# Optimization experiments

Measured on AMD Instinct MI355X. Metric: run time of the kernel, lower is better.

Reference implementation:

```python
import jax, jax.numpy as jnp
import numpy as np

B, N_IN, N_OUT = 8192, 2048, 2048


def setup_inputs() -> dict:
    key = jax.random.key(0)
    kx, kw = jax.random.split(key)
    x = jax.random.normal(kx, (B, N_IN), dtype=jnp.float32)
    # torch: uniform_(-0.5, 0.5)
    weight = jax.random.uniform(kw, (N_IN, N_OUT), dtype=jnp.float32, minval=-0.5, maxval=0.5)
    return {"x": x, "weight": weight}


def reference(x, weight):
    # Binarize: W > 0 -> {0, 1}; then dense matmul (batch, n_in) @ (n_in, n_out)
    w_bin = (weight > 0).astype(x.dtype)
    return x @ w_bin
```

## Files before the change

kernel.cpp:

```cpp
#include <hip/hip_runtime.h>


#define MDIM 8192
#define NDIM 2048
#define KDIM 2048
#define NT   (KDIM / 128)
#define CH   (64 * KDIM)

typedef __attribute__((ext_vector_type(8))) short short8;
typedef __attribute__((ext_vector_type(4))) float float4v;
typedef __attribute__((ext_vector_type(4))) float f32x4;
typedef __attribute__((ext_vector_type(4))) int int4v;
typedef __attribute__((ext_vector_type(4))) unsigned short ushort4v;
typedef __attribute__((ext_vector_type(8))) unsigned short ushort8v;

__device__ __forceinline__ unsigned short f2bf(float f) {
    union { float f; unsigned u; } v; v.f = f;
    unsigned r = v.u + 0x7FFFu + ((v.u >> 16) & 1u);
    return (unsigned short)(r >> 16);
}

__device__ __forceinline__ void gload_lds16(void* l, const void* g) {
    __builtin_amdgcn_global_load_lds(
        (const __attribute__((address_space(1))) unsigned int*)g,
        (__attribute__((address_space(3))) unsigned int*)l,
        16, 0, 0);
}

#define FENCE asm volatile("" ::: "memory")
#define BAR do { FENCE; __builtin_amdgcn_s_barrier(); FENCE; } while (0)

__global__ __launch_bounds__(256) void prep(const float* __restrict__ X,
                                            const float* __restrict__ W,
                                            signed char* __restrict__ Xq,
                                            signed char* __restrict__ Wt,
                                            float* __restrict__ Sc) {
    __shared__ __align__(16) signed char T[64][80];
    __shared__ float wm[4];
    const int t = threadIdx.x;
    const int bid = blockIdx.x;

    if (bid < MDIM) {
        const int row = bid;
        const float* xr = X + (size_t)row * KDIM + t * 8;
        float4v a = *reinterpret_cast<const float4v*>(xr);
        float4v b = *reinterpret_cast<const float4v*>(xr + 4);
        float m = fabsf(a[0]);
        m = fmaxf(m, fabsf(a[1])); m = fmaxf(m, fabsf(a[2])); m = fmaxf(m, fabsf(a[3]));
        m = fmaxf(m, fabsf(b[0])); m = fmaxf(m, fabsf(b[1]));
        m = fmaxf(m, fabsf(b[2])); m = fmaxf(m, fabsf(b[3]));
#pragma unroll
        for (int off = 32; off; off >>= 1)
            m = fmaxf(m, __shfl_xor(m, off));
        if ((t & 63) == 0) wm[t >> 6] = m;
        __syncthreads();
        const float s = fmaxf(fmaxf(wm[0], wm[1]), fmaxf(wm[2], wm[3]));
        const float inv = (s > 0.f) ? 127.0f / s : 0.f;

        int q[8];
        q[0] = __float2int_rn(a[0] * inv); q[1] = __float2int_rn(a[1] * inv);
        q[2] = __float2int_rn(a[2] * inv); q[3] = __float2int_rn(a[3] * inv);
        q[4] = __float2int_rn(b[0] * inv); q[5] = __float2int_rn(b[1] * inv);
        q[6] = __float2int_rn(b[2] * inv); q[7] = __float2int_rn(b[3] * inv);
        unsigned lo = (q[0] & 255) | ((q[1] & 255) << 8) | ((q[2] & 255) << 16) | ((unsigned)(q[3] & 255) << 24);
        unsigned hi = (q[4] & 255) | ((q[5] & 255) << 8) | ((q[6] & 255) << 16) | ((unsigned)(q[7] & 255) << 24);
        unsigned* dst = (unsigned*)(Xq + (size_t)row * KDIM + t * 8);
        dst[0] = lo; dst[1] = hi;
        if (t == 0) Sc[row] = s * (1.0f / 127.0f);
    } else {
        const int wb = bid - MDIM;
        const int k0 = (wb >> 5) * 64;
        const int n0 = (wb & 31) * 64;
        const int kr = t >> 4;
        const int nc = (t & 15) * 4;
#pragma unroll
        for (int rr = 0; rr < 4; ++rr) {
            int k = k0 + rr * 16 + kr;
            float4v w4 = *reinterpret_cast<const float4v*>(W + (size_t)k * NDIM + n0 + nc);
#pragma unroll
            for (int c = 0; c < 4; ++c)
                T[nc + c][rr * 16 + kr] = (w4[c] > 0.0f) ? (signed char)1 : (signed char)0;
        }
        __syncthreads();
        const int row = t >> 2, ch = t & 3;
        int4v v = *reinterpret_cast<const int4v*>(&T[row][ch * 16]);
        *reinterpret_cast<int4v*>(Wt + (size_t)(n0 + row) * KDIM + k0 + ch * 16) = v;
    }
}

__global__ __launch_bounds__(512, 1) void gemm_i8(const signed char* __restrict__ A,
                                                  const signed char* __restrict__ Bt,
                                                  const float* __restrict__ Sc,
                                                  float* __restrict__ O) {
    extern __shared__ char lds[];
    const int tid  = threadIdx.x;
    const int lane = tid & 63;
    const int w    = tid >> 6;
    const int wr   = w >> 2;
    const int wc   = w & 3;

    int id  = blockIdx.x;
    int swz = (id & 7) * 32 + (id >> 3);
    const int bm = swz >> 3;
    const int bn = swz & 7;

    const int l3 = lane >> 3, l7 = lane & 7;
    const int srcOff = (w * 8 + l3) * KDIM + ((l7 ^ l3) << 4);
    const char* gA = (const char*)A + (size_t)(bm * 256) * KDIM + srcOff;
    const char* gB = (const char*)Bt + (size_t)(bn * 256) * KDIM + srcOff;

    const int fr = lane & 15, fg = lane >> 4;
    const int se0 = ((fg)     ^ (fr & 7)) << 4;
    const int se1 = ((4 + fg) ^ (fr & 7)) << 4;
    const int aRd = (wr * 128 + fr) * 128;
    const int bRd = 32768 + (wc * 64 + fr) * 128;

    int4v acc[8][4];
#pragma unroll
    for (int i = 0; i < 8; ++i)
#pragma unroll
        for (int j = 0; j < 4; ++j) {
            acc[i][j][0] = 0; acc[i][j][1] = 0; acc[i][j][2] = 0; acc[i][j][3] = 0;
        }

    gload_lds16(lds + 32768 + 0 * 8192 + w * 1024, gB + 0 * CH);
    gload_lds16(lds + 32768 + 2 * 8192 + w * 1024, gB + 2 * CH);
    gload_lds16(lds + 32768 + 1 * 8192 + w * 1024, gB + 1 * CH);
    gload_lds16(lds + 32768 + 3 * 8192 + w * 1024, gB + 3 * CH);
    gload_lds16(lds + 0 * 8192 + w * 1024, gA + 0 * CH);
    gload_lds16(lds + 2 * 8192 + w * 1024, gA + 2 * CH);
    gload_lds16(lds + 1 * 8192 + w * 1024, gA + 1 * CH);
    gload_lds16(lds + 3 * 8192 + w * 1024, gA + 3 * CH);
    asm volatile("s_waitcnt vmcnt(0)" ::: "memory");
    BAR;

    int4v af[4][2], bfr[4][2];

    for (int t = 0; t < NT; ++t) {
        const int cur = (t & 1) << 16;
        const int nxt = ((t + 1) & 1) << 16;
        const bool more = (t + 1 < NT);
        const char* gAs = gA + (size_t)(t + 1) * 128;
        const char* gBs = gB + (size_t)(t + 1) * 128;

        asm volatile("s_waitcnt vmcnt(2)" ::: "memory");
        BAR;
#pragma unroll
        for (int j = 0; j < 4; ++j) {
            af[j][0] = *reinterpret_cast<const int4v*>(lds + cur + aRd + j * 2048 + se0);
            af[j][1] = *reinterpret_cast<const int4v*>(lds + cur + aRd + j * 2048 + se1);
        }
#pragma unroll
        for (int n = 0; n < 4; ++n) {
            bfr[n][0] = *reinterpret_cast<const int4v*>(lds + cur + bRd + n * 2048 + se0);
            bfr[n][1] = *reinterpret_cast<const int4v*>(lds + cur + bRd + n * 2048 + se1);
        }
        if (more) {
            gload_lds16(lds + nxt + 32768 + 0 * 8192 + w * 1024, gBs + 0 * CH);
            gload_lds16(lds + nxt + 32768 + 2 * 8192 + w * 1024, gBs + 2 * CH);
            gload_lds16(lds + nxt + 32768 + 1 * 8192 + w * 1024, gBs + 1 * CH);
            gload_lds16(lds + nxt + 32768 + 3 * 8192 + w * 1024, gBs + 3 * CH);
        }
        __builtin_amdgcn_s_setprio(1);
#pragma unroll
        for (int mi = 0; mi < 4; ++mi)
#pragma unroll
            for (int ni = 0; ni < 4; ++ni) {
                acc[mi][ni] = __builtin_amdgcn_mfma_i32_16x16x64_i8(
                    af[mi][0], bfr[ni][0], acc[mi][ni], 0, 0, 0);
                acc[mi][ni] = __builtin_amdgcn_mfma_i32_16x16x64_i8(
                    af[mi][1], bfr[ni][1], acc[mi][ni], 0, 0, 0);
            }
        __builtin_amdgcn_s_setprio(0);

        if (more) asm volatile("s_waitcnt vmcnt(4)" ::: "memory");
        else      asm volatile("s_waitcnt vmcnt(0)" ::: "memory");
        BAR;
#pragma unroll
        for (int j = 0; j < 4; ++j) {
            af[j][0] = *reinterpret_cast<const int4v*>(lds + cur + aRd + (4 + j) * 2048 + se0);
            af[j][1] = *reinterpret_cast<const int4v*>(lds + cur + aRd + (4 + j) * 2048 + se1);
        }
        if (more) {
            gload_lds16(lds + nxt + 0 * 8192 + w * 1024, gAs + 0 * CH);
            gload_lds16(lds + nxt + 2 * 8192 + w * 1024, gAs + 2 * CH);
            gload_lds16(lds + nxt + 1 * 8192 + w * 1024, gAs + 1 * CH);
            gload_lds16(lds + nxt + 3 * 8192 + w * 1024, gAs + 3 * CH);
        }
        __builtin_amdgcn_s_setprio(1);
#pragma unroll
        for (int mi = 0; mi < 4; ++mi)
#pragma unroll
            for (int ni = 0; ni < 4; ++ni) {
                acc[4 + mi][ni] = __builtin_amdgcn_mfma_i32_16x16x64_i8(
                    af[mi][0], bfr[ni][0], acc[4 + mi][ni], 0, 0, 0);
                acc[4 + mi][ni] = __builtin_amdgcn_mfma_i32_16x16x64_i8(
                    af[mi][1], bfr[ni][1], acc[4 + mi][ni], 0, 0, 0);
            }
        __builtin_amdgcn_s_setprio(0);
    }

    const int orow0 = bm * 256 + wr * 128 + fg * 4;
    const int ocol0 = bn * 256 + wc * 64 + fr;
#pragma unroll
    for (int mi = 0; mi < 8; ++mi)
#pragma unroll
        for (int r = 0; r < 4; ++r) {
            const int row = orow0 + mi * 16 + r;
            const float s = Sc[row];
            float* op = O + (size_t)row * NDIM + ocol0;
#pragma unroll
            for (int ni = 0; ni < 4; ++ni)
                op[ni * 16] = s * (float)acc[mi][ni][r];
        }
}

__global__ __launch_bounds__(256, 2) void binlin_fused(
        const float* __restrict__ X, const float* __restrict__ W,
        float* __restrict__ O) {
    const int tid = threadIdx.x;
    const int lane = tid & 63;
    const int wave = tid >> 6;
    const int wr = wave >> 1, wc = wave & 1;
    const int NWG = (MDIM / 128) * (NDIM / 128);
    int id = blockIdx.x;
    int swz = (id & 7) * (NWG >> 3) + (id >> 3);
    const int bm = swz >> 4, bn = swz & 15;

    __shared__ __align__(16) unsigned short As[128][40];
    __shared__ __align__(16) unsigned short Bs[128][40];

    const int rA = tid >> 3, kA = (tid & 7) * 4;
    const float* aPtr = X + (size_t)(bm * 128 + rA) * KDIM + kA;
    const int nB = (tid & 31) * 4, kB = (tid >> 5) * 4;
    const float* bPtr = W + (size_t)kB * NDIM + (size_t)bn * 128 + nB;

    float4v aReg[4], bReg[4];
#pragma unroll
    for (int p = 0; p < 4; ++p)
        aReg[p] = *reinterpret_cast<const float4v*>(aPtr + (size_t)(32 * p) * KDIM);
#pragma unroll
    for (int dk = 0; dk < 4; ++dk)
        bReg[dk] = *reinterpret_cast<const float4v*>(bPtr + (size_t)dk * NDIM);

    f32x4 acc[4][4];
#pragma unroll
    for (int i = 0; i < 4; ++i)
#pragma unroll
        for (int j = 0; j < 4; ++j) {
            acc[i][j][0] = 0.f; acc[i][j][1] = 0.f; acc[i][j][2] = 0.f; acc[i][j][3] = 0.f;
        }

    const int r16 = lane & 15, g8 = (lane >> 4) * 8;
    for (int kt = 0; kt < KDIM; kt += 32) {
#pragma unroll
        for (int p = 0; p < 4; ++p) {
            ushort4v v;
            v[0] = f2bf(aReg[p][0]); v[1] = f2bf(aReg[p][1]);
            v[2] = f2bf(aReg[p][2]); v[3] = f2bf(aReg[p][3]);
            *reinterpret_cast<ushort4v*>(&As[rA + 32 * p][kA]) = v;
        }
        unsigned short bb[4][4];
#pragma unroll
        for (int dk = 0; dk < 4; ++dk)
#pragma unroll
            for (int dn = 0; dn < 4; ++dn)
                bb[dn][dk] = (bReg[dk][dn] > 0.0f) ? (unsigned short)0x3F80u
                                                   : (unsigned short)0u;
#pragma unroll
        for (int dn = 0; dn < 4; ++dn) {
            ushort4v v;
            v[0] = bb[dn][0]; v[1] = bb[dn][1]; v[2] = bb[dn][2]; v[3] = bb[dn][3];
            *reinterpret_cast<ushort4v*>(&Bs[nB + dn][kB]) = v;
        }
        __syncthreads();
        if (kt + 32 < KDIM) {
#pragma unroll
            for (int p = 0; p < 4; ++p)
                aReg[p] = *reinterpret_cast<const float4v*>(
                    aPtr + (size_t)(32 * p) * KDIM + (kt + 32));
#pragma unroll
            for (int dk = 0; dk < 4; ++dk)
                bReg[dk] = *reinterpret_cast<const float4v*>(
                    bPtr + (size_t)(kt + 32 + dk) * NDIM);
        }
        short8 af[4], bf[4];
#pragma unroll
        for (int mi = 0; mi < 4; ++mi)
            af[mi] = *reinterpret_cast<const short8*>(&As[wr * 64 + mi * 16 + r16][g8]);
#pragma unroll
        for (int ni = 0; ni < 4; ++ni)
            bf[ni] = *reinterpret_cast<const short8*>(&Bs[wc * 64 + ni * 16 + r16][g8]);
#pragma unroll
        for (int mi = 0; mi < 4; ++mi)
#pragma unroll
            for (int ni = 0; ni < 4; ++ni)
                acc[mi][ni] = __builtin_amdgcn_mfma_f32_16x16x32_bf16(
                    af[mi], bf[ni], acc[mi][ni], 0, 0, 0);
        __syncthreads();
    }

    const int orow0 = bm * 128 + wr * 64 + (lane >> 4) * 4;
    const int ocol0 = bn * 128 + wc * 64 + r16;
#pragma unroll
    for (int mi = 0; mi < 4; ++mi)
#pragma unroll
        for (int ni = 0; ni < 4; ++ni)
#pragma unroll
            for (int r = 0; r < 4; ++r)
                O[(size_t)(orow0 + mi * 16 + r) * NDIM + ocol0 + ni * 16] =
                    acc[mi][ni][r];
}

extern "C" void kernel_launch(void* const* d_in, const int* in_sizes, int n_in,
                              void* d_out, int out_size, void* d_ws, size_t ws_size,
                              hipStream_t stream) {
    const float* X = (const float*)d_in[0];
    const float* W = (const float*)d_in[1];
    float* O = (float*)d_out;
    (void)in_sizes; (void)n_in; (void)out_size;

    const size_t xq_bytes = (size_t)MDIM * KDIM;
    const size_t wt_bytes = (size_t)NDIM * KDIM;
    const size_t sc_bytes = (size_t)MDIM * sizeof(float);
    const size_t need = xq_bytes + wt_bytes + sc_bytes;

    if (ws_size >= need) {
        signed char* Xq = (signed char*)d_ws;
        signed char* Wt = Xq + xq_bytes;
        float* Sc = (float*)(Wt + wt_bytes);
        hipFuncSetAttribute((const void*)gemm_i8,
                            hipFuncAttributeMaxDynamicSharedMemorySize, 131072);
        prep<<<dim3(MDIM + (KDIM / 64) * (NDIM / 64)), dim3(256), 0, stream>>>(X, W, Xq, Wt, Sc);
        gemm_i8<<<dim3((MDIM / 256) * (NDIM / 256)), dim3(512), 131072, stream>>>(Xq, Wt, Sc, O);
    } else {
        binlin_fused<<<dim3((MDIM / 128) * (NDIM / 128)), dim3(256), 0, stream>>>(X, W, O);
    }
}
```

Baseline: 55.80 us.

## Restructure int8 GEMM main loop into single-barrier prefetch with staged A fragments

```diff
diff --git a/kernel.cpp b/kernel.cpp
--- a/kernel.cpp
+++ b/kernel.cpp
@@ -88,7 +88,7 @@
     }
 }
 
-__global__ __launch_bounds__(512, 1) void gemm_i8(const signed char* __restrict__ A,
+__global__ __launch_bounds__(512, 2) void gemm_i8(const signed char* __restrict__ A,
                                                   const signed char* __restrict__ Bt,
                                                   const float* __restrict__ Sc,
                                                   float* __restrict__ O) {
@@ -124,17 +124,13 @@
         }
 
     gload_lds16(lds + 32768 + 0 * 8192 + w * 1024, gB + 0 * CH);
+    gload_lds16(lds + 32768 + 1 * 8192 + w * 1024, gB + 1 * CH);
     gload_lds16(lds + 32768 + 2 * 8192 + w * 1024, gB + 2 * CH);
-    gload_lds16(lds + 32768 + 1 * 8192 + w * 1024, gB + 1 * CH);
     gload_lds16(lds + 32768 + 3 * 8192 + w * 1024, gB + 3 * CH);
     gload_lds16(lds + 0 * 8192 + w * 1024, gA + 0 * CH);
+    gload_lds16(lds + 1 * 8192 + w * 1024, gA + 1 * CH);
     gload_lds16(lds + 2 * 8192 + w * 1024, gA + 2 * CH);
-    gload_lds16(lds + 1 * 8192 + w * 1024, gA + 1 * CH);
     gload_lds16(lds + 3 * 8192 + w * 1024, gA + 3 * CH);
-    asm volatile("s_waitcnt vmcnt(0)" ::: "memory");
-    BAR;
-
-    int4v af[4][2], bfr[4][2];
 
     for (int t = 0; t < NT; ++t) {
         const int cur = (t & 1) << 16;
@@ -143,59 +139,78 @@
         const char* gAs = gA + (size_t)(t + 1) * 128;
         const char* gBs = gB + (size_t)(t + 1) * 128;
 
-        asm volatile("s_waitcnt vmcnt(2)" ::: "memory");
+        asm volatile("s_waitcnt vmcnt(0)" ::: "memory");
         BAR;
-#pragma unroll
-        for (int j = 0; j < 4; ++j) {
-            af[j][0] = *reinterpret_cast<const int4v*>(lds + cur + aRd + j * 2048 + se0);
-            af[j][1] = *reinterpret_cast<const int4v*>(lds + cur + aRd + j * 2048 + se1);
-        }
+
+        if (more) {
+            gload_lds16(lds + nxt + 32768 + 0 * 8192 + w * 1024, gBs + 0 * CH);
+            gload_lds16(lds + nxt + 32768 + 1 * 8192 + w * 1024, gBs + 1 * CH);
+            gload_lds16(lds + nxt + 32768 + 2 * 8192 + w * 1024, gBs + 2 * CH);
+            gload_lds16(lds + nxt + 32768 + 3 * 8192 + w * 1024, gBs + 3 * CH);
+            gload_lds16(lds + nxt + 0 * 8192 + w * 1024, gAs + 0 * CH);
+            gload_lds16(lds + nxt + 1 * 8192 + w * 1024, gAs + 1 * CH);
+            gload_lds16(lds + nxt + 2 * 8192 + w * 1024, gAs + 2 * CH);
+            gload_lds16(lds + nxt + 3 * 8192 + w * 1024, gAs + 3 * CH);
+        }
+
+        int4v bfr[4][2], a01[2][2], a23[2][2], a45[2][2], a67[2][2];
 #pragma unroll
         for (int n = 0; n < 4; ++n) {
             bfr[n][0] = *reinterpret_cast<const int4v*>(lds + cur + bRd + n * 2048 + se0);
             bfr[n][1] = *reinterpret_cast<const int4v*>(lds + cur + bRd + n * 2048 + se1);
         }
-        if (more) {
-            gload_lds16(lds + nxt + 32768 + 0 * 8192 + w * 1024, gBs + 0 * CH);
-            gload_lds16(lds + nxt + 32768 + 2 * 8192 + w * 1024, gBs + 2 * CH);
-            gload_lds16(lds + nxt + 32768 + 1 * 8192 + w * 1024, gBs + 1 * CH);
-            gload_lds16(lds + nxt + 32768 + 3 * 8192 + w * 1024, gBs + 3 * CH);
+#pragma unroll
+        for (int d = 0; d < 2; ++d) {
+            a01[d][0] = *reinterpret_cast<const int4v*>(lds + cur + aRd + d * 2048 + se0);
+            a01[d][1] = *reinterpret_cast<const int4v*>(lds + cur + aRd + d * 2048 + se1);
+        }
+#pragma unroll
+        for (int d = 0; d < 2; ++d) {
+            a23[d][0] = *reinterpret_cast<const int4v*>(lds + cur + aRd + (2 + d) * 2048 + se0);
+            a23[d][1] = *reinterpret_cast<const int4v*>(lds + cur + aRd + (2 + d) * 2048 + se1);
         }
         __builtin_amdgcn_s_setprio(1);
 #pragma unroll
-        for (int mi = 0; mi < 4; ++mi)
+        for (int d = 0; d < 2; ++d)
 #pragma unroll
             for (int ni = 0; ni < 4; ++ni) {
-                acc[mi][ni] = __builtin_amdgcn_mfma_i32_16x16x64_i8(
-                    af[mi][0], bfr[ni][0], acc[mi][ni], 0, 0, 0);
-                acc[mi][ni] = __builtin_amdgcn_mfma_i32_16x16x64_i8(
-                    af[mi][1], bfr[ni][1], acc[mi][ni], 0, 0, 0);
+                acc[d][ni] = __builtin_amdgcn_mfma_i32_16x16x64_i8(a01[d][0], bfr[ni][0], acc[d][ni], 0, 0, 0);
+                acc[d][ni] = __builtin_amdgcn_mfma_i32_16x16x64_i8(a01[d][1], bfr[ni][1], acc[d][ni], 0, 0, 0);
             }
         __builtin_amdgcn_s_setprio(0);
-
-        if (more) asm volatile("s_waitcnt vmcnt(4)" ::: "memory");
-        else      asm volatile("s_waitcnt vmcnt(0)" ::: "memory");
-        BAR;
-#pragma unroll
-        for (int j = 0; j < 4; ++j) {
-            af[j][0] = *reinterpret_cast<const int4v*>(lds + cur + aRd + (4 + j) * 2048 + se0);
-            af[j][1] = *reinterpret_cast<const int4v*>(lds + cur + aRd + (4 + j) * 2048 + se1);
-        }
-        if (more) {
-            gload_lds16(lds + nxt + 0 * 8192 + w * 1024, gAs + 0 * CH);
-            gload_lds16(lds + nxt + 2 * 8192 + w * 1024, gAs + 2 * CH);
-            gload_lds16(lds + nxt + 1 * 8192 + w * 1024, gAs + 1 * CH);
-            gload_lds16(lds + nxt + 3 * 8192 + w * 1024, gAs + 3 * CH);
+#pragma unroll
+        for (int d = 0; d < 2; ++d) {
+            a45[d][0] = *reinterpret_cast<const int4v*>(lds + cur + aRd + (4 + d) * 2048 + se0);
+            a45[d][1] = *reinterpret_cast<const int4v*>(lds + cur + aRd + (4 + d) * 2048 + se1);
         }
         __builtin_amdgcn_s_setprio(1);
 #pragma unroll
-        for (int mi = 0; mi < 4; ++mi)
+        for (int d = 0; d < 2; ++d)
 #pragma unroll
             for (int ni = 0; ni < 4; ++ni) {
-                acc[4 + mi][ni] = __builtin_amdgcn_mfma_i32_16x16x64_i8(
-                    af[mi][0], bfr[ni][0], acc[4 + mi][ni], 0, 0, 0);
-                acc[4 + mi][ni] = __builtin_amdgcn_mfma_i32_16x16x64_i8(
-                    af[mi][1], bfr[ni][1], acc[4 + mi][ni], 0, 0, 0);
+                acc[2 + d][ni] = __builtin_amdgcn_mfma_i32_16x16x64_i8(a23[d][0], bfr[ni][0], acc[2 + d][ni], 0, 0, 0);
+                acc[2 + d][ni] = __builtin_amdgcn_mfma_i32_16x16x64_i8(a23[d][1], bfr[ni][1], acc[2 + d][ni], 0, 0, 0);
+            }
+        __builtin_amdgcn_s_setprio(0);
+#pragma unroll
+        for (int d = 0; d < 2; ++d) {
+            a67[d][0] = *reinterpret_cast<const int4v*>(lds + cur + aRd + (6 + d) * 2048 + se0);
+            a67[d][1] = *reinterpret_cast<const int4v*>(lds + cur + aRd + (6 + d) * 2048 + se1);
+        }
+        __builtin_amdgcn_s_setprio(1);
+#pragma unroll
+        for (int d = 0; d < 2; ++d)
+#pragma unroll
+            for (int ni = 0; ni < 4; ++ni) {
+                acc[4 + d][ni] = __builtin_amdgcn_mfma_i32_16x16x64_i8(a45[d][0], bfr[ni][0], acc[4 + d][ni], 0, 0, 0);
+                acc[4 + d][ni] = __builtin_amdgcn_mfma_i32_16x16x64_i8(a45[d][1], bfr[ni][1], acc[4 + d][ni], 0, 0, 0);
+            }
+#pragma unroll
+        for (int d = 0; d < 2; ++d)
+#pragma unroll
+            for (int ni = 0; ni < 4; ++ni) {
+                acc[6 + d][ni] = __builtin_amdgcn_mfma_i32_16x16x64_i8(a67[d][0], bfr[ni][0], acc[6 + d][ni], 0, 0, 0);
+                acc[6 + d][ni] = __builtin_amdgcn_mfma_i32_16x16x64_i8(a67[d][1], bfr[ni][1], acc[6 + d][ni], 0, 0, 0);
             }
         __builtin_amdgcn_s_setprio(0);
     }
```

Result: no change. 56.10 us (+0.5%).

## Shrink int8 GEMM tile to 128x128 with 4 waves, two blocks per CU

Applied to the files above, without the earlier changes.

```diff
diff --git a/kernel.cpp b/kernel.cpp
--- a/kernel.cpp
+++ b/kernel.cpp
@@ -5,7 +5,6 @@
 #define NDIM 2048
 #define KDIM 2048
 #define NT   (KDIM / 128)
-#define CH   (64 * KDIM)
 
 typedef __attribute__((ext_vector_type(8))) short short8;
 typedef __attribute__((ext_vector_type(4))) float float4v;
@@ -88,7 +87,7 @@
     }
 }
 
-__global__ __launch_bounds__(512, 1) void gemm_i8(const signed char* __restrict__ A,
+__global__ __launch_bounds__(256, 2) void gemm128(const signed char* __restrict__ A,
                                                   const signed char* __restrict__ Bt,
                                                   const float* __restrict__ Sc,
                                                   float* __restrict__ O) {
@@ -96,114 +95,85 @@
     const int tid  = threadIdx.x;
     const int lane = tid & 63;
     const int w    = tid >> 6;
-    const int wr   = w >> 2;
-    const int wc   = w & 3;
+    const int wm_  = w >> 1;
+    const int wn_  = w & 1;
 
     int id  = blockIdx.x;
-    int swz = (id & 7) * 32 + (id >> 3);
-    const int bm = swz >> 3;
-    const int bn = swz & 7;
+    int swz = (id & 7) * 128 + (id >> 3);
+    const int bm = swz >> 4;
+    const int bn = swz & 15;
 
     const int l3 = lane >> 3, l7 = lane & 7;
     const int srcOff = (w * 8 + l3) * KDIM + ((l7 ^ l3) << 4);
-    const char* gA = (const char*)A + (size_t)(bm * 256) * KDIM + srcOff;
-    const char* gB = (const char*)Bt + (size_t)(bn * 256) * KDIM + srcOff;
+    const char* gA = (const char*)A + (size_t)(bm * 128) * KDIM + srcOff;
+    const char* gB = (const char*)Bt + (size_t)(bn * 128) * KDIM + srcOff;
 
     const int fr = lane & 15, fg = lane >> 4;
     const int se0 = ((fg)     ^ (fr & 7)) << 4;
     const int se1 = ((4 + fg) ^ (fr & 7)) << 4;
-    const int aRd = (wr * 128 + fr) * 128;
-    const int bRd = 32768 + (wc * 64 + fr) * 128;
-
-    int4v acc[8][4];
-#pragma unroll
-    for (int i = 0; i < 8; ++i)
+    const int aRd = (wm_ * 64 + fr) * 128;
+    const int bRd = 16384 + (wn_ * 64 + fr) * 128;
+
+    int4v acc[4][4];
+#pragma unroll
+    for (int i = 0; i < 4; ++i)
 #pragma unroll
         for (int j = 0; j < 4; ++j) {
             acc[i][j][0] = 0; acc[i][j][1] = 0; acc[i][j][2] = 0; acc[i][j][3] = 0;
         }
 
-    gload_lds16(lds + 32768 + 0 * 8192 + w * 1024, gB + 0 * CH);
-    gload_lds16(lds + 32768 + 2 * 8192 + w * 1024, gB + 2 * CH);
-    gload_lds16(lds + 32768 + 1 * 8192 + w * 1024, gB + 1 * CH);
-    gload_lds16(lds + 32768 + 3 * 8192 + w * 1024, gB + 3 * CH);
-    gload_lds16(lds + 0 * 8192 + w * 1024, gA + 0 * CH);
-    gload_lds16(lds + 2 * 8192 + w * 1024, gA + 2 * CH);
-    gload_lds16(lds + 1 * 8192 + w * 1024, gA + 1 * CH);
-    gload_lds16(lds + 3 * 8192 + w * 1024, gA + 3 * CH);
-    asm volatile("s_waitcnt vmcnt(0)" ::: "memory");
-    BAR;
-
-    int4v af[4][2], bfr[4][2];
+#pragma unroll
+    for (int i = 0; i < 4; ++i)
+        gload_lds16(lds + i * 4096 + w * 1024, gA + (size_t)i * 32 * KDIM);
+#pragma unroll
+    for (int i = 0; i < 4; ++i)
+        gload_lds16(lds + 16384 + i * 4096 + w * 1024, gB + (size_t)i * 32 * KDIM);
 
     for (int t = 0; t < NT; ++t) {
-        const int cur = (t & 1) << 16;
-        const int nxt = ((t + 1) & 1) << 16;
+        const int cur = (t & 1) << 15;
+        const int nxt = ((t + 1) & 1) << 15;
         const bool more = (t + 1 < NT);
         const char* gAs = gA + (size_t)(t + 1) * 128;
         const char* gBs = gB + (size_t)(t + 1) * 128;
 
-        asm volatile("s_waitcnt vmcnt(2)" ::: "memory");
+        asm volatile("s_waitcnt vmcnt(0)" ::: "memory");
         BAR;
-#pragma unroll
-        for (int j = 0; j < 4; ++j) {
-            af[j][0] = *reinterpret_cast<const int4v*>(lds + cur + aRd + j * 2048 + se0);
-            af[j][1] = *reinterpret_cast<const int4v*>(lds + cur + aRd + j * 2048 + se1);
-        }
+
+        if (more) {
+#pragma unroll
+            for (int i = 0; i < 4; ++i)
+                gload_lds16(lds + nxt + i * 4096 + w * 1024, gAs + (size_t)i * 32 * KDIM);
+#pragma unroll
+            for (int i = 0; i < 4; ++i)
+                gload_lds16(lds + nxt + 16384 + i * 4096 + w * 1024, gBs + (size_t)i * 32 * KDIM);
+        }
+
+        int4v bfr[4][2], af[4][2];
 #pragma unroll
         for (int n = 0; n < 4; ++n) {
             bfr[n][0] = *reinterpret_cast<const int4v*>(lds + cur + bRd + n * 2048 + se0);
             bfr[n][1] = *reinterpret_cast<const int4v*>(lds + cur + bRd + n * 2048 + se1);
         }
-        if (more) {
-            gload_lds16(lds + nxt + 32768 + 0 * 8192 + w * 1024, gBs + 0 * CH);
-            gload_lds16(lds + nxt + 32768 + 2 * 8192 + w * 1024, gBs + 2 * CH);
-            gload_lds16(lds + nxt + 32768 + 1 * 8192 + w * 1024, gBs + 1 * CH);
-            gload_lds16(lds + nxt + 32768 + 3 * 8192 + w * 1024, gBs + 3 * CH);
+#pragma unroll
+        for (int m = 0; m < 4; ++m) {
+            af[m][0] = *reinterpret_cast<const int4v*>(lds + cur + aRd + m * 2048 + se0);
+            af[m][1] = *reinterpret_cast<const int4v*>(lds + cur + aRd + m * 2048 + se1);
         }
         __builtin_amdgcn_s_setprio(1);
 #pragma unroll
-        for (int mi = 0; mi < 4; ++mi)
-#pragma unroll
-            for (int ni = 0; ni < 4; ++ni) {
-                acc[mi][ni] = __builtin_amdgcn_mfma_i32_16x16x64_i8(
-                    af[mi][0], bfr[ni][0], acc[mi][ni], 0, 0, 0);
-                acc[mi][ni] = __builtin_amdgcn_mfma_i32_16x16x64_i8(
-                    af[mi][1], bfr[ni][1], acc[mi][ni], 0, 0, 0);
-            }
-        __builtin_amdgcn_s_setprio(0);
-
-        if (more) asm volatile("s_waitcnt vmcnt(4)" ::: "memory");
-        else      asm volatile("s_waitcnt vmcnt(0)" ::: "memory");
-        BAR;
-#pragma unroll
-        for (int j = 0; j < 4; ++j) {
-            af[j][0] = *reinterpret_cast<const int4v*>(lds + cur + aRd + (4 + j) * 2048 + se0);
-            af[j][1] = *reinterpret_cast<const int4v*>(lds + cur + aRd + (4 + j) * 2048 + se1);
-        }
-        if (more) {
-            gload_lds16(lds + nxt + 0 * 8192 + w * 1024, gAs + 0 * CH);
-            gload_lds16(lds + nxt + 2 * 8192 + w * 1024, gAs + 2 * CH);
-            gload_lds16(lds + nxt + 1 * 8192 + w * 1024, gAs + 1 * CH);
-            gload_lds16(lds + nxt + 3 * 8192 + w * 1024, gAs + 3 * CH);
-        }
-        __builtin_amdgcn_s_setprio(1);
-#pragma unroll
-        for (int mi = 0; mi < 4; ++mi)
-#pragma unroll
-            for (int ni = 0; ni < 4; ++ni) {
-                acc[4 + mi][ni] = __builtin_amdgcn_mfma_i32_16x16x64_i8(
-                    af[mi][0], bfr[ni][0], acc[4 + mi][ni], 0, 0, 0);
-                acc[4 + mi][ni] = __builtin_amdgcn_mfma_i32_16x16x64_i8(
-                    af[mi][1], bfr[ni][1], acc[4 + mi][ni], 0, 0, 0);
+        for (int m = 0; m < 4; ++m)
+#pragma unroll
+            for (int n = 0; n < 4; ++n) {
+                acc[m][n] = __builtin_amdgcn_mfma_i32_16x16x64_i8(af[m][0], bfr[n][0], acc[m][n], 0, 0, 0);
+                acc[m][n] = __builtin_amdgcn_mfma_i32_16x16x64_i8(af[m][1], bfr[n][1], acc[m][n], 0, 0, 0);
             }
         __builtin_amdgcn_s_setprio(0);
     }
 
-    const int orow0 = bm * 256 + wr * 128 + fg * 4;
-    const int ocol0 = bn * 256 + wc * 64 + fr;
-#pragma unroll
-    for (int mi = 0; mi < 8; ++mi)
+    const int orow0 = bm * 128 + wm_ * 64 + fg * 4;
+    const int ocol0 = bn * 128 + wn_ * 64 + fr;
+#pragma unroll
+    for (int mi = 0; mi < 4; ++mi)
 #pragma unroll
         for (int r = 0; r < 4; ++r) {
             const int row = orow0 + mi * 16 + r;
@@ -329,10 +299,10 @@
         signed char* Xq = (signed char*)d_ws;
         signed char* Wt = Xq + xq_bytes;
         float* Sc = (float*)(Wt + wt_bytes);
-        hipFuncSetAttribute((const void*)gemm_i8,
-                            hipFuncAttributeMaxDynamicSharedMemorySize, 131072);
+        hipFuncSetAttribute((const void*)gemm128,
+                            hipFuncAttributeMaxDynamicSharedMemorySize, 65536);
         prep<<<dim3(MDIM + (KDIM / 64) * (NDIM / 64)), dim3(256), 0, stream>>>(X, W, Xq, Wt, Sc);
-        gemm_i8<<<dim3((MDIM / 256) * (NDIM / 256)), dim3(512), 131072, stream>>>(Xq, Wt, Sc, O);
+        gemm128<<<dim3((MDIM / 128) * (NDIM / 128)), dim3(256), 65536, stream>>>(Xq, Wt, Sc, O);
     } else {
         binlin_fused<<<dim3((MDIM / 128) * (NDIM / 128)), dim3(256), 0, stream>>>(X, W, O);
     }
```

Result: slower. 58.38 us (+4.6%).
